# Kernel optimization log

Measured on AMD Instinct MI355X. Metric: run time of the kernel, lower is better.

Reference implementation:

```python
import jax, jax.numpy as jnp
import numpy as np

DIM = 768
NUM_HEADS = 12
MLP_RATIO = 4.0
HIDDEN = int(DIM * MLP_RATIO)
EPS = 1e-6  # flax LayerNorm default


def setup_inputs() -> dict:
    key = jax.random.key(0)
    ks = jax.random.split(key, 8)
    d = DIM
    init = lambda k, shape, fan_in: jax.random.normal(k, shape, jnp.float32) * (fan_in ** -0.5)
    return {
        "x": jax.random.normal(ks[0], (8, 1024, d), jnp.float32),
        "ln1_scale": jnp.ones((d,), jnp.float32),
        "ln1_bias": jnp.zeros((d,), jnp.float32),
        "qkv_w": init(ks[1], (d, 3 * d), d),
        "qkv_b": jnp.zeros((3 * d,), jnp.float32),
        "proj_w": init(ks[2], (d, d), d),
        "proj_b": jnp.zeros((d,), jnp.float32),
        "ln2_scale": jnp.ones((d,), jnp.float32),
        "ln2_bias": jnp.zeros((d,), jnp.float32),
        "fc1_w": init(ks[3], (d, HIDDEN), d),
        "fc1_b": jnp.zeros((HIDDEN,), jnp.float32),
        "fc2_w": init(ks[4], (HIDDEN, d), HIDDEN),
        "fc2_b": jnp.zeros((d,), jnp.float32),
    }


def _layernorm(x, scale, bias):
    mu = jnp.mean(x, axis=-1, keepdims=True)
    var = jnp.mean(jnp.square(x - mu), axis=-1, keepdims=True)
    return (x - mu) * jax.lax.rsqrt(var + EPS) * scale + bias


def reference(x, ln1_scale, ln1_bias, qkv_w, qkv_b, proj_w, proj_b,
              ln2_scale, ln2_bias, fc1_w, fc1_b, fc2_w, fc2_b):
    b, n, d = x.shape
    h = NUM_HEADS
    hd = d // h
    scale = hd ** -0.5

    # --- attention (pre-norm) ---
    y = _layernorm(x, ln1_scale, ln1_bias)
    qkv = y @ qkv_w + qkv_b                      # [b, n, 3d]
    qkv = qkv.reshape(b, n, 3, h, hd).transpose(2, 0, 3, 1, 4)  # [3, b, h, n, hd]
    q, k, v = qkv[0], qkv[1], qkv[2]
    attn = jnp.einsum("bhqd,bhkd->bhqk", q, k) * scale
    attn = jax.nn.softmax(attn, axis=-1)
    o = jnp.einsum("bhqk,bhkd->bhqd", attn, v)   # [b, h, n, hd]
    o = o.transpose(0, 2, 1, 3).reshape(b, n, d)
    x = x + (o @ proj_w + proj_b)

    # --- MLP (pre-norm) ---
    y = _layernorm(x, ln2_scale, ln2_bias)
    y = jax.nn.gelu(y @ fc1_w + fc1_b)
    x = x + (y @ fc2_w + fc2_b)
    return x
```

## Files before the change

### kernel.cpp

```cpp
#include <hip/hip_runtime.h>
#include <hip/hip_bf16.h>
#include <math.h>


#define DIM 768
#define SEQ 1024
#define BATCH 8
#define NHEAD 12
#define HDIM 64
#define HID 3072
#define MTOK (BATCH * SEQ)

typedef __attribute__((ext_vector_type(8))) short short8;
typedef __attribute__((ext_vector_type(4))) short short4v;
typedef __attribute__((ext_vector_type(4))) float floatx4;

__device__ __forceinline__ short f2s(float x) {
  __hip_bfloat16 h = __float2bfloat16(x);
  return __builtin_bit_cast(short, h);
}
__device__ __forceinline__ float s2f(short s) {
  return __bfloat162float(__builtin_bit_cast(__hip_bfloat16, s));
}
__device__ __forceinline__ floatx4 zf4() {
  floatx4 v; v[0] = v[1] = v[2] = v[3] = 0.f; return v;
}
__device__ __forceinline__ float gelu_f(float x) {
  float z = 0.7978845608028654f * (x + 0.044715f * x * x * x);
  float u = __expf(2.f * z);
  return 0.5f * x * (2.f - 2.f / (u + 1.f));
}

__global__ __launch_bounds__(256) void pre_kernel(
    const float* __restrict__ w0, short* __restrict__ o0,
    const float* __restrict__ w1, short* __restrict__ o1,
    const float* __restrict__ w2, short* __restrict__ o2,
    const float* __restrict__ w3, short* __restrict__ o3,
    const float* __restrict__ x, const float* __restrict__ ls,
    const float* __restrict__ lb, short* __restrict__ y) {
  const int id = blockIdx.x;
  const int t = threadIdx.x;
  if (id < 6912) {
    __shared__ float tile[32][33];
    const float* in;
    short* out;
    int K, N, tid;
    if (id < 1728)      { in = w0; out = o0; K = DIM; N = 3 * DIM; tid = id; }
    else if (id < 2304) { in = w1; out = o1; K = DIM; N = DIM;     tid = id - 1728; }
    else if (id < 4608) { in = w2; out = o2; K = DIM; N = HID;     tid = id - 2304; }
    else                { in = w3; out = o3; K = HID; N = DIM;     tid = id - 4608; }
    const int ntx = N >> 5;
    const int n0 = (tid % ntx) * 32, k0 = (tid / ntx) * 32;
    const int tx = t & 31, ty = t >> 5;
#pragma unroll
    for (int i = 0; i < 4; ++i)
      tile[ty + i * 8][tx] = in[(size_t)(k0 + ty + i * 8) * N + n0 + tx];
    __syncthreads();
#pragma unroll
    for (int i = 0; i < 4; ++i)
      out[(size_t)(n0 + ty + i * 8) * K + k0 + tx] = f2s(tile[tx][ty + i * 8]);
  } else {
    const int row = id - 6912;
    const float* xr = x + (size_t)row * DIM;
    float v[3];
    float s1 = 0.f, s2 = 0.f;
#pragma unroll
    for (int j = 0; j < 3; ++j) {
      v[j] = xr[t + j * 256];
      s1 += v[j];
      s2 += v[j] * v[j];
    }
#pragma unroll
    for (int off = 32; off; off >>= 1) {
      s1 += __shfl_down(s1, off, 64);
      s2 += __shfl_down(s2, off, 64);
    }
    __shared__ float r1[4], r2[4], bc[2];
    const int wave = t >> 6, lane = t & 63;
    if (lane == 0) { r1[wave] = s1; r2[wave] = s2; }
    __syncthreads();
    if (t == 0) {
      float S1 = r1[0] + r1[1] + r1[2] + r1[3];
      float S2 = r2[0] + r2[1] + r2[2] + r2[3];
      float mu = S1 * (1.0f / DIM);
      float var = S2 * (1.0f / DIM) - mu * mu;
      bc[0] = mu;
      bc[1] = rsqrtf(fmaxf(var, 0.f) + 1e-6f);
    }
    __syncthreads();
    const float mu = bc[0], rstd = bc[1];
#pragma unroll
    for (int j = 0; j < 3; ++j) {
      const int idx = t + j * 256;
      y[(size_t)row * DIM + idx] = f2s((v[j] - mu) * rstd * ls[idx] + lb[idx]);
    }
  }
}

__global__ __launch_bounds__(256) void ln_kernel(const float* __restrict__ x,
                                                 const float* __restrict__ scale,
                                                 const float* __restrict__ bias,
                                                 short* __restrict__ y) {
  const int row = blockIdx.x;
  const int t = threadIdx.x;
  const float* xr = x + (size_t)row * DIM;
  float v[3];
  float s1 = 0.f, s2 = 0.f;
#pragma unroll
  for (int j = 0; j < 3; ++j) {
    v[j] = xr[t + j * 256];
    s1 += v[j];
    s2 += v[j] * v[j];
  }
#pragma unroll
  for (int off = 32; off; off >>= 1) {
    s1 += __shfl_down(s1, off, 64);
    s2 += __shfl_down(s2, off, 64);
  }
  __shared__ float r1[4], r2[4], bc[2];
  const int wave = t >> 6, lane = t & 63;
  if (lane == 0) { r1[wave] = s1; r2[wave] = s2; }
  __syncthreads();
  if (t == 0) {
    float S1 = r1[0] + r1[1] + r1[2] + r1[3];
    float S2 = r2[0] + r2[1] + r2[2] + r2[3];
    float mu = S1 * (1.0f / DIM);
    float var = S2 * (1.0f / DIM) - mu * mu;
    bc[0] = mu;
    bc[1] = rsqrtf(fmaxf(var, 0.f) + 1e-6f);
  }
  __syncthreads();
  const float mu = bc[0], rstd = bc[1];
#pragma unroll
  for (int j = 0; j < 3; ++j) {
    const int idx = t + j * 256;
    y[(size_t)row * DIM + idx] = f2s((v[j] - mu) * rstd * scale[idx] + bias[idx]);
  }
}

template <int ROWS, int THREADS>
__device__ __forceinline__ void stageT(const short* __restrict__ src, int ld,
                                       short* lds, int t) {
#pragma unroll
  for (int i = 0; i < (ROWS * 4) / THREADS; ++i) {
    const int S = i * THREADS + t;
    const int row = S >> 2;
    const int chunk = (S & 3) ^ ((row >> 1) & 3);
    const short* g = src + (size_t)row * ld + chunk * 8;
    const unsigned off = __builtin_amdgcn_readfirstlane((unsigned)((S & ~63) * 16));
    __builtin_amdgcn_global_load_lds(
        (const __attribute__((address_space(1))) void*)g,
        (__attribute__((address_space(3))) void*)((char*)lds + off), 16, 0, 0);
  }
}

template <int MODE>
__global__ __launch_bounds__(256) void gemm_w192(
    const short* __restrict__ A, const short* __restrict__ Bt,
    const float* __restrict__ bias,
    short* __restrict__ outB,
    short* __restrict__ Qb, short* __restrict__ Kb, short* __restrict__ Vtb,
    int N, int K) {
  __shared__ __align__(16) short Asm[4][4096];
  __shared__ __align__(16) short Bsm[4][6144];
  const int t = threadIdx.x;
  const int lane = t & 63, w = t >> 6, quad = lane >> 4, l15 = lane & 15;

  const int nbx = gridDim.x;
  const int lid = blockIdx.y * nbx + blockIdx.x;
  const int xcd = lid & 7, local = lid >> 3;
  const int m0 = ((local / nbx) * 8 + xcd) * 128;
  const int n0 = (local % nbx) * 192;
  const int mb = (w & 1) * 64, nb = (w >> 1) * 96;

  floatx4 acc[4][6];
#pragma unroll
  for (int mi = 0; mi < 4; ++mi)
#pragma unroll
    for (int ni = 0; ni < 6; ++ni) acc[mi][ni] = zf4();

  const short* Ab = A + (size_t)m0 * K;
  const short* Bb = Bt + (size_t)n0 * K;
  const int nk = K >> 5;

  stageT<128, 256>(Ab, K, Asm[0], t);       stageT<192, 256>(Bb, K, Bsm[0], t);
  stageT<128, 256>(Ab + 32, K, Asm[1], t);  stageT<192, 256>(Bb + 32, K, Bsm[1], t);
  stageT<128, 256>(Ab + 64, K, Asm[2], t);  stageT<192, 256>(Bb + 64, K, Bsm[2], t);

#define W192_STEP(BUF) do { \
  short8 a_[4], b_[6]; \
  _Pragma("unroll") for (int mi = 0; mi < 4; ++mi) { \
    const int r = mb + mi * 16 + l15; \
    a_[mi] = *(const short8*)(Asm[BUF] + r * 32 + ((quad ^ ((r >> 1) & 3)) * 8)); \
  } \
  _Pragma("unroll") for (int ni = 0; ni < 6; ++ni) { \
    const int r = nb + ni * 16 + l15; \
    b_[ni] = *(const short8*)(Bsm[BUF] + r * 32 + ((quad ^ ((r >> 1) & 3)) * 8)); \
  } \
  _Pragma("unroll") for (int mi = 0; mi < 4; ++mi) \
    _Pragma("unroll") for (int ni = 0; ni < 6; ++ni) \
      acc[mi][ni] = __builtin_amdgcn_mfma_f32_16x16x32_bf16(a_[mi], b_[ni], acc[mi][ni], 0, 0, 0); \
} while (0)

#define W192_IT(J, BUF, NXT) do { \
  if ((J) + 2 < nk)      asm volatile("s_waitcnt vmcnt(10)" ::: "memory"); \
  else if ((J) + 1 < nk) asm volatile("s_waitcnt vmcnt(5)" ::: "memory"); \
  else                   asm volatile("s_waitcnt vmcnt(0)" ::: "memory"); \
  __builtin_amdgcn_s_barrier(); \
  if ((J) + 3 < nk) { \
    stageT<128, 256>(Ab + ((J) + 3) * 32, K, Asm[NXT], t); \
    stageT<192, 256>(Bb + ((J) + 3) * 32, K, Bsm[NXT], t); \
  } \
  W192_STEP(BUF); \
} while (0)

  for (int kt = 0; kt < nk; kt += 4) {
    W192_IT(kt + 0, 0, 3);
    W192_IT(kt + 1, 1, 0);
    W192_IT(kt + 2, 2, 1);
    W192_IT(kt + 3, 3, 2);
  }

#pragma unroll
  for (int mi = 0; mi < 4; ++mi) {
    const int row0 = m0 + mb + mi * 16 + quad * 4;
#pragma unroll
    for (int ni = 0; ni < 6; ++ni) {
      const int col = n0 + nb + ni * 16 + l15;
      const float bv = bias[col];
      float v[4];
#pragma unroll
      for (int r = 0; r < 4; ++r) v[r] = acc[mi][ni][r] + bv;
      if (MODE == 0) {
        const int bb = row0 >> 10;
        const int s0 = row0 & 1023;
        if (col < 1536) {
          const int cc = (col < 768) ? col : col - 768;
          const int h = cc >> 6, d = cc & 63;
          short* dst = (col < 768 ? Qb : Kb) + (size_t)(bb * NHEAD + h) * SEQ * HDIM;
#pragma unroll
          for (int r = 0; r < 4; ++r) dst[(size_t)(s0 + r) * HDIM + d] = f2s(v[r]);
        } else {
          const int cc = col - 1536;
          const int h = cc >> 6, d = cc & 63;
          short4v pv;
#pragma unroll
          for (int r = 0; r < 4; ++r) pv[r] = f2s(v[r]);
          *(short4v*)(Vtb + ((size_t)(bb * NHEAD + h) * HDIM + d) * SEQ + s0) = pv;
        }
      } else {
#pragma unroll
        for (int r = 0; r < 4; ++r)
          outB[(size_t)(row0 + r) * N + col] = f2s(gelu_f(v[r]));
      }
    }
  }
}

__global__ __launch_bounds__(128) void gemm_n64(
    const short* __restrict__ A, const short* __restrict__ Bt,
    const float* __restrict__ bias, const float* __restrict__ res,
    float* __restrict__ outF, int N, int K) {
  __shared__ __align__(16) short Asm[4][4096];
  __shared__ __align__(16) short Bsm[4][2048];
  const int t = threadIdx.x;
  const int lane = t & 63, w = t >> 6, quad = lane >> 4, l15 = lane & 15;

  const int nbx = gridDim.x;
  const int lid = blockIdx.y * nbx + blockIdx.x;
  const int xcd = lid & 7, local = lid >> 3;
  const int m0 = ((local / nbx) * 8 + xcd) * 128;
  const int n0 = (local % nbx) * 64;
  const int mb = w * 64;

  floatx4 acc[4][4];
#pragma unroll
  for (int mi = 0; mi < 4; ++mi)
#pragma unroll
    for (int ni = 0; ni < 4; ++ni) acc[mi][ni] = zf4();

  const short* Ab = A + (size_t)m0 * K;
  const short* Bb = Bt + (size_t)n0 * K;
  const int nk = K >> 5;

  stageT<128, 128>(Ab, K, Asm[0], t);       stageT<64, 128>(Bb, K, Bsm[0], t);
  stageT<128, 128>(Ab + 32, K, Asm[1], t);  stageT<64, 128>(Bb + 32, K, Bsm[1], t);
  stageT<128, 128>(Ab + 64, K, Asm[2], t);  stageT<64, 128>(Bb + 64, K, Bsm[2], t);

#define N64_STEP(BUF) do { \
  short8 a_[4], b_[4]; \
  _Pragma("unroll") for (int mi = 0; mi < 4; ++mi) { \
    const int r = mb + mi * 16 + l15; \
    a_[mi] = *(const short8*)(Asm[BUF] + r * 32 + ((quad ^ ((r >> 1) & 3)) * 8)); \
  } \
  _Pragma("unroll") for (int ni = 0; ni < 4; ++ni) { \
    const int r = ni * 16 + l15; \
    b_[ni] = *(const short8*)(Bsm[BUF] + r * 32 + ((quad ^ ((r >> 1) & 3)) * 8)); \
  } \
  _Pragma("unroll") for (int mi = 0; mi < 4; ++mi) \
    _Pragma("unroll") for (int ni = 0; ni < 4; ++ni) \
      acc[mi][ni] = __builtin_amdgcn_mfma_f32_16x16x32_bf16(a_[mi], b_[ni], acc[mi][ni], 0, 0, 0); \
} while (0)

#define N64_IT(J, BUF, NXT) do { \
  if ((J) + 2 < nk)      asm volatile("s_waitcnt vmcnt(12)" ::: "memory"); \
  else if ((J) + 1 < nk) asm volatile("s_waitcnt vmcnt(6)" ::: "memory"); \
  else                   asm volatile("s_waitcnt vmcnt(0)" ::: "memory"); \
  __builtin_amdgcn_s_barrier(); \
  if ((J) + 3 < nk) { \
    stageT<128, 128>(Ab + ((J) + 3) * 32, K, Asm[NXT], t); \
    stageT<64, 128>(Bb + ((J) + 3) * 32, K, Bsm[NXT], t); \
  } \
  N64_STEP(BUF); \
} while (0)

  for (int kt = 0; kt < nk; kt += 4) {
    N64_IT(kt + 0, 0, 3);
    N64_IT(kt + 1, 1, 0);
    N64_IT(kt + 2, 2, 1);
    N64_IT(kt + 3, 3, 2);
  }

#pragma unroll
  for (int mi = 0; mi < 4; ++mi) {
    const int row0 = m0 + mb + mi * 16 + quad * 4;
#pragma unroll
    for (int ni = 0; ni < 4; ++ni) {
      const int col = n0 + ni * 16 + l15;
      const float bv = bias[col];
#pragma unroll
      for (int r = 0; r < 4; ++r) {
        const size_t idx = (size_t)(row0 + r) * N + col;
        outF[idx] = acc[mi][ni][r] + bv + res[idx];
      }
    }
  }
}

__device__ __forceinline__ void stage64(const short* __restrict__ src, int ld,
                                        short* lds, int t) {
  const int lane = t & 63, w = t >> 6;
#pragma unroll
  for (int i = 0; i < 2; ++i) {
    const int S = w * 128 + i * 64 + lane;
    const int r = S >> 3, c0 = S & 7;
    const int c = c0 ^ (r & 7);
    const short* g = src + (size_t)r * ld + c * 8;
    const unsigned off = __builtin_amdgcn_readfirstlane((unsigned)((w * 128 + i * 64) * 16));
    __builtin_amdgcn_global_load_lds(
        (const __attribute__((address_space(1))) void*)g,
        (__attribute__((address_space(3))) void*)((char*)lds + off), 16, 0, 0);
  }
}

__global__ __launch_bounds__(256) void attn_kernel(
    const short* __restrict__ Qb, const short* __restrict__ Kb,
    const short* __restrict__ Vtb, short* __restrict__ o) {
  __shared__ __align__(16) short Ks[2][4096];
  __shared__ __align__(16) short Vts[2][4096];
  __shared__ __align__(16) short Pt[8192];
  const int t = threadIdx.x;
  const int lane = t & 63, w = t >> 6, quad = lane >> 4, l15 = lane & 15;
  const int bh = blockIdx.x;
  const int q0 = blockIdx.y * 128;
  const size_t qkbase = (size_t)bh * SEQ * HDIM;
  const size_t vbase = (size_t)bh * HDIM * SEQ;
  short* ptw = Pt + w * 2048;
  const float cexp = 0.18033688011f;

  short8 bq[2][2];
#pragma unroll
  for (int mi = 0; mi < 2; ++mi)
#pragma unroll
    for (int ks = 0; ks < 2; ++ks)
      bq[mi][ks] = *(const short8*)(Qb + qkbase +
                                    (size_t)(q0 + w * 32 + mi * 16 + l15) * HDIM +
                                    ks * 32 + quad * 8);

  floatx4 oacc[4][2];
  float l_acc[2] = {0.f, 0.f};
#pragma unroll
  for (int di = 0; di < 4; ++di)
#pragma unroll
    for (int mi = 0; mi < 2; ++mi) oacc[di][mi] = zf4();

  stage64(Kb + qkbase, HDIM, Ks[0], t);
  stage64(Vtb + vbase, SEQ, Vts[0], t);

  for (int kt = 0; kt < 16; ++kt) {
    __syncthreads();
    const int cur = kt & 1;
    if (kt < 15) {
      stage64(Kb + qkbase + (size_t)(kt + 1) * 64 * HDIM, HDIM, Ks[cur ^ 1], t);
      stage64(Vtb + vbase + (kt + 1) * 64, SEQ, Vts[cur ^ 1], t);
    }

    floatx4 sacc[4][2];
#pragma unroll
    for (int ni = 0; ni < 4; ++ni)
#pragma unroll
      for (int mi = 0; mi < 2; ++mi) sacc[ni][mi] = zf4();
#pragma unroll
    for (int ks = 0; ks < 2; ++ks) {
      short8 ak[4];
#pragma unroll
      for (int ni = 0; ni < 4; ++ni) {
        const int r = ni * 16 + l15;
        ak[ni] = *(const short8*)(Ks[cur] + r * 64 + (((ks * 4 + quad) ^ (r & 7)) * 8));
      }
#pragma unroll
      for (int ni = 0; ni < 4; ++ni)
#pragma unroll
        for (int mi = 0; mi < 2; ++mi)
          sacc[ni][mi] = __builtin_amdgcn_mfma_f32_16x16x32_bf16(ak[ni], bq[mi][ks], sacc[ni][mi], 0, 0, 0);
    }

#pragma unroll
    for (int mi = 0; mi < 2; ++mi) {
      const int row = mi * 16 + l15;
      const int swz = (row & 7) ^ ((row & 8) >> 1);
#pragma unroll
      for (int ni = 0; ni < 4; ++ni) {
        short4v pk;
#pragma unroll
        for (int r = 0; r < 4; ++r) {
          const float p = exp2f(sacc[ni][mi][r] * cexp);
          l_acc[mi] += p;
          pk[r] = f2s(p);
        }
        const int c = ni * 2 + (quad >> 1);
        *(short4v*)(ptw + row * 64 + ((c ^ swz) * 8 + (quad & 1) * 4)) = pk;
      }
    }

#pragma unroll
    for (int ks = 0; ks < 2; ++ks) {
      short8 bp[2];
#pragma unroll
      for (int mi = 0; mi < 2; ++mi) {
        const int row = mi * 16 + l15;
        const int swz = (row & 7) ^ ((row & 8) >> 1);
        bp[mi] = *(const short8*)(ptw + row * 64 + (((ks * 4 + quad) ^ swz) * 8));
      }
      short8 av[4];
#pragma unroll
      for (int di = 0; di < 4; ++di) {
        const int r = di * 16 + l15;
        av[di] = *(const short8*)(Vts[cur] + r * 64 + (((ks * 4 + quad) ^ (r & 7)) * 8));
      }
#pragma unroll
      for (int di = 0; di < 4; ++di)
#pragma unroll
        for (int mi = 0; mi < 2; ++mi)
          oacc[di][mi] = __builtin_amdgcn_mfma_f32_16x16x32_bf16(av[di], bp[mi], oacc[di][mi], 0, 0, 0);
    }
  }

  const int bb = bh / NHEAD, hh = bh % NHEAD;
  float inv[2];
#pragma unroll
  for (int mi = 0; mi < 2; ++mi) {
    float l = l_acc[mi];
    l += __shfl_xor(l, 16, 64);
    l += __shfl_xor(l, 32, 64);
    inv[mi] = 1.0f / l;
  }
#pragma unroll
  for (int di = 0; di < 4; ++di)
#pragma unroll
    for (int mi = 0; mi < 2; ++mi) {
      const int tok = bb * SEQ + q0 + w * 32 + mi * 16 + l15;
      const int d = hh * HDIM + di * 16 + quad * 4;
      short4v ov;
#pragma unroll
      for (int r = 0; r < 4; ++r) ov[r] = f2s(oacc[di][mi][r] * inv[mi]);
      *(short4v*)(o + (size_t)tok * DIM + d) = ov;
    }
}

extern "C" void kernel_launch(void* const* d_in, const int* in_sizes, int n_in,
                              void* d_out, int out_size, void* d_ws, size_t ws_size,
                              hipStream_t stream) {
  const float* x      = (const float*)d_in[0];
  const float* ln1_s  = (const float*)d_in[1];
  const float* ln1_b  = (const float*)d_in[2];
  const float* qkv_w  = (const float*)d_in[3];
  const float* qkv_b  = (const float*)d_in[4];
  const float* proj_w = (const float*)d_in[5];
  const float* proj_b = (const float*)d_in[6];
  const float* ln2_s  = (const float*)d_in[7];
  const float* ln2_b  = (const float*)d_in[8];
  const float* fc1_w  = (const float*)d_in[9];
  const float* fc1_b  = (const float*)d_in[10];
  const float* fc2_w  = (const float*)d_in[11];
  const float* fc2_b  = (const float*)d_in[12];
  float* out = (float*)d_out;

  char* p = (char*)d_ws;
  short* wqt = (short*)p; p += (size_t)(3 * DIM) * DIM * 2;
  short* wpt = (short*)p; p += (size_t)DIM * DIM * 2;
  short* w1t = (short*)p; p += (size_t)HID * DIM * 2;
  short* w2t = (short*)p; p += (size_t)DIM * HID * 2;
  short* y   = (short*)p; p += (size_t)MTOK * DIM * 2;
  short* Qb  = (short*)p; p += (size_t)MTOK * DIM * 2;
  short* Kb  = (short*)p; p += (size_t)MTOK * DIM * 2;
  short* Vtb = (short*)p; p += (size_t)MTOK * DIM * 2;
  float* x1  = (float*)p; p += (size_t)MTOK * DIM * 4;
  short* h   = (short*)p; p += (size_t)MTOK * HID * 2;
  short* obuf = y;
  short* y2   = Qb;

  pre_kernel<<<6912 + MTOK, 256, 0, stream>>>(qkv_w, wqt, proj_w, wpt, fc1_w, w1t,
                                              fc2_w, w2t, x, ln1_s, ln1_b, y);
  gemm_w192<0><<<dim3(12, 64), 256, 0, stream>>>(
      y, wqt, qkv_b, nullptr, Qb, Kb, Vtb, 3 * DIM, DIM);
  attn_kernel<<<dim3(BATCH * NHEAD, SEQ / 128), 256, 0, stream>>>(Qb, Kb, Vtb, obuf);
  gemm_n64<<<dim3(12, 64), 128, 0, stream>>>(
      obuf, wpt, proj_b, x, x1, DIM, DIM);
  ln_kernel<<<MTOK, 256, 0, stream>>>(x1, ln2_s, ln2_b, y2);
  gemm_w192<2><<<dim3(16, 64), 256, 0, stream>>>(
      y2, w1t, fc1_b, h, nullptr, nullptr, nullptr, HID, DIM);
  gemm_n64<<<dim3(12, 64), 128, 0, stream>>>(
      h, w2t, fc2_b, x1, out, DIM, HID);
}
```

Before: 423.1 us.

## Replace LDS-staged GEMM pipelines with direct global-to-register double buffering

Both GEMM kernels drop the four-stage global_load_lds shared-memory pipeline and barriers. Each wave now loads its MFMA fragments directly from global memory into registers, double-buffered across k-steps. This removes LDS usage and block-level synchronization, which may raise occupancy. In exchange, operand tiles shared between waves are fetched redundantly from global/L2, and memory latency is hidden only by a two-deep register prefetch.

```diff
diff --git a/kernel.cpp b/kernel.cpp
--- a/kernel.cpp
+++ b/kernel.cpp
@@ -138,31 +138,13 @@
   }
 }
 
-template <int ROWS, int THREADS>
-__device__ __forceinline__ void stageT(const short* __restrict__ src, int ld,
-                                       short* lds, int t) {
-#pragma unroll
-  for (int i = 0; i < (ROWS * 4) / THREADS; ++i) {
-    const int S = i * THREADS + t;
-    const int row = S >> 2;
-    const int chunk = (S & 3) ^ ((row >> 1) & 3);
-    const short* g = src + (size_t)row * ld + chunk * 8;
-    const unsigned off = __builtin_amdgcn_readfirstlane((unsigned)((S & ~63) * 16));
-    __builtin_amdgcn_global_load_lds(
-        (const __attribute__((address_space(1))) void*)g,
-        (__attribute__((address_space(3))) void*)((char*)lds + off), 16, 0, 0);
-  }
-}
-
 template <int MODE>
-__global__ __launch_bounds__(256) void gemm_w192(
+__global__ __launch_bounds__(256) void gemm_reg192(
     const short* __restrict__ A, const short* __restrict__ Bt,
     const float* __restrict__ bias,
     short* __restrict__ outB,
     short* __restrict__ Qb, short* __restrict__ Kb, short* __restrict__ Vtb,
     int N, int K) {
-  __shared__ __align__(16) short Asm[4][4096];
-  __shared__ __align__(16) short Bsm[4][6144];
   const int t = threadIdx.x;
   const int lane = t & 63, w = t >> 6, quad = lane >> 4, l15 = lane & 15;
 
@@ -173,52 +155,42 @@
   const int n0 = (local % nbx) * 192;
   const int mb = (w & 1) * 64, nb = (w >> 1) * 96;
 
+  const short* pa[4];
+  const short* pb[6];
+#pragma unroll
+  for (int mi = 0; mi < 4; ++mi)
+    pa[mi] = A + (size_t)(m0 + mb + mi * 16 + l15) * K + quad * 8;
+#pragma unroll
+  for (int ni = 0; ni < 6; ++ni)
+    pb[ni] = Bt + (size_t)(n0 + nb + ni * 16 + l15) * K + quad * 8;
+
   floatx4 acc[4][6];
 #pragma unroll
   for (int mi = 0; mi < 4; ++mi)
 #pragma unroll
     for (int ni = 0; ni < 6; ++ni) acc[mi][ni] = zf4();
 
-  const short* Ab = A + (size_t)m0 * K;
-  const short* Bb = Bt + (size_t)n0 * K;
-  const int nk = K >> 5;
-
-  stageT<128, 256>(Ab, K, Asm[0], t);       stageT<192, 256>(Bb, K, Bsm[0], t);
-  stageT<128, 256>(Ab + 32, K, Asm[1], t);  stageT<192, 256>(Bb + 32, K, Bsm[1], t);
-  stageT<128, 256>(Ab + 64, K, Asm[2], t);  stageT<192, 256>(Bb + 64, K, Bsm[2], t);
-
-#define W192_STEP(BUF) do { \
-  short8 a_[4], b_[6]; \
-  _Pragma("unroll") for (int mi = 0; mi < 4; ++mi) { \
-    const int r = mb + mi * 16 + l15; \
-    a_[mi] = *(const short8*)(Asm[BUF] + r * 32 + ((quad ^ ((r >> 1) & 3)) * 8)); \
-  } \
-  _Pragma("unroll") for (int ni = 0; ni < 6; ++ni) { \
-    const int r = nb + ni * 16 + l15; \
-    b_[ni] = *(const short8*)(Bsm[BUF] + r * 32 + ((quad ^ ((r >> 1) & 3)) * 8)); \
-  } \
+#define R192_LOAD(AD, BD, KOFF) do { \
+  _Pragma("unroll") for (int mi = 0; mi < 4; ++mi) \
+    AD[mi] = *(const short8*)(pa[mi] + (KOFF)); \
+  _Pragma("unroll") for (int ni = 0; ni < 6; ++ni) \
+    BD[ni] = *(const short8*)(pb[ni] + (KOFF)); \
+} while (0)
+
+#define R192_MFMA(AD, BD) do { \
   _Pragma("unroll") for (int mi = 0; mi < 4; ++mi) \
     _Pragma("unroll") for (int ni = 0; ni < 6; ++ni) \
-      acc[mi][ni] = __builtin_amdgcn_mfma_f32_16x16x32_bf16(a_[mi], b_[ni], acc[mi][ni], 0, 0, 0); \
+      acc[mi][ni] = __builtin_amdgcn_mfma_f32_16x16x32_bf16(AD[mi], BD[ni], acc[mi][ni], 0, 0, 0); \
 } while (0)
 
-#define W192_IT(J, BUF, NXT) do { \
-  if ((J) + 2 < nk)      asm volatile("s_waitcnt vmcnt(10)" ::: "memory"); \
-  else if ((J) + 1 < nk) asm volatile("s_waitcnt vmcnt(5)" ::: "memory"); \
-  else                   asm volatile("s_waitcnt vmcnt(0)" ::: "memory"); \
-  __builtin_amdgcn_s_barrier(); \
-  if ((J) + 3 < nk) { \
-    stageT<128, 256>(Ab + ((J) + 3) * 32, K, Asm[NXT], t); \
-    stageT<192, 256>(Bb + ((J) + 3) * 32, K, Bsm[NXT], t); \
-  } \
-  W192_STEP(BUF); \
-} while (0)
-
-  for (int kt = 0; kt < nk; kt += 4) {
-    W192_IT(kt + 0, 0, 3);
-    W192_IT(kt + 1, 1, 0);
-    W192_IT(kt + 2, 2, 1);
-    W192_IT(kt + 3, 3, 2);
+  short8 a0[4], b0[6], a1[4], b1[6];
+  R192_LOAD(a0, b0, 0);
+  const int nk = K >> 5;
+  for (int kt = 0; kt < nk; kt += 2) {
+    R192_LOAD(a1, b1, (kt + 1) * 32);
+    R192_MFMA(a0, b0);
+    if (kt + 2 < nk) R192_LOAD(a0, b0, (kt + 2) * 32);
+    R192_MFMA(a1, b1);
   }
 
 #pragma unroll
@@ -257,12 +229,10 @@
   }
 }
 
-__global__ __launch_bounds__(128) void gemm_n64(
+__global__ __launch_bounds__(128) void gemm_reg64(
     const short* __restrict__ A, const short* __restrict__ Bt,
     const float* __restrict__ bias, const float* __restrict__ res,
     float* __restrict__ outF, int N, int K) {
-  __shared__ __align__(16) short Asm[4][4096];
-  __shared__ __align__(16) short Bsm[4][2048];
   const int t = threadIdx.x;
   const int lane = t & 63, w = t >> 6, quad = lane >> 4, l15 = lane & 15;
 
@@ -273,52 +243,42 @@
   const int n0 = (local % nbx) * 64;
   const int mb = w * 64;
 
+  const short* pa[4];
+  const short* pb[4];
+#pragma unroll
+  for (int mi = 0; mi < 4; ++mi)
+    pa[mi] = A + (size_t)(m0 + mb + mi * 16 + l15) * K + quad * 8;
+#pragma unroll
+  for (int ni = 0; ni < 4; ++ni)
+    pb[ni] = Bt + (size_t)(n0 + ni * 16 + l15) * K + quad * 8;
+
   floatx4 acc[4][4];
 #pragma unroll
   for (int mi = 0; mi < 4; ++mi)
 #pragma unroll
     for (int ni = 0; ni < 4; ++ni) acc[mi][ni] = zf4();
 
-  const short* Ab = A + (size_t)m0 * K;
-  const short* Bb = Bt + (size_t)n0 * K;
-  const int nk = K >> 5;
-
-  stageT<128, 128>(Ab, K, Asm[0], t);       stageT<64, 128>(Bb, K, Bsm[0], t);
-  stageT<128, 128>(Ab + 32, K, Asm[1], t);  stageT<64, 128>(Bb + 32, K, Bsm[1], t);
-  stageT<128, 128>(Ab + 64, K, Asm[2], t);  stageT<64, 128>(Bb + 64, K, Bsm[2], t);
-
-#define N64_STEP(BUF) do { \
-  short8 a_[4], b_[4]; \
-  _Pragma("unroll") for (int mi = 0; mi < 4; ++mi) { \
-    const int r = mb + mi * 16 + l15; \
-    a_[mi] = *(const short8*)(Asm[BUF] + r * 32 + ((quad ^ ((r >> 1) & 3)) * 8)); \
-  } \
-  _Pragma("unroll") for (int ni = 0; ni < 4; ++ni) { \
-    const int r = ni * 16 + l15; \
-    b_[ni] = *(const short8*)(Bsm[BUF] + r * 32 + ((quad ^ ((r >> 1) & 3)) * 8)); \
-  } \
+#define R64_LOAD(AD, BD, KOFF) do { \
+  _Pragma("unroll") for (int mi = 0; mi < 4; ++mi) \
+    AD[mi] = *(const short8*)(pa[mi] + (KOFF)); \
+  _Pragma("unroll") for (int ni = 0; ni < 4; ++ni) \
+    BD[ni] = *(const short8*)(pb[ni] + (KOFF)); \
+} while (0)
+
+#define R64_MFMA(AD, BD) do { \
   _Pragma("unroll") for (int mi = 0; mi < 4; ++mi) \
     _Pragma("unroll") for (int ni = 0; ni < 4; ++ni) \
-      acc[mi][ni] = __builtin_amdgcn_mfma_f32_16x16x32_bf16(a_[mi], b_[ni], acc[mi][ni], 0, 0, 0); \
+      acc[mi][ni] = __builtin_amdgcn_mfma_f32_16x16x32_bf16(AD[mi], BD[ni], acc[mi][ni], 0, 0, 0); \
 } while (0)
 
-#define N64_IT(J, BUF, NXT) do { \
-  if ((J) + 2 < nk)      asm volatile("s_waitcnt vmcnt(12)" ::: "memory"); \
-  else if ((J) + 1 < nk) asm volatile("s_waitcnt vmcnt(6)" ::: "memory"); \
-  else                   asm volatile("s_waitcnt vmcnt(0)" ::: "memory"); \
-  __builtin_amdgcn_s_barrier(); \
-  if ((J) + 3 < nk) { \
-    stageT<128, 128>(Ab + ((J) + 3) * 32, K, Asm[NXT], t); \
-    stageT<64, 128>(Bb + ((J) + 3) * 32, K, Bsm[NXT], t); \
-  } \
-  N64_STEP(BUF); \
-} while (0)
-
-  for (int kt = 0; kt < nk; kt += 4) {
-    N64_IT(kt + 0, 0, 3);
-    N64_IT(kt + 1, 1, 0);
-    N64_IT(kt + 2, 2, 1);
-    N64_IT(kt + 3, 3, 2);
+  short8 a0[4], b0[4], a1[4], b1[4];
+  R64_LOAD(a0, b0, 0);
+  const int nk = K >> 5;
+  for (int kt = 0; kt < nk; kt += 2) {
+    R64_LOAD(a1, b1, (kt + 1) * 32);
+    R64_MFMA(a0, b0);
+    if (kt + 2 < nk) R64_LOAD(a0, b0, (kt + 2) * 32);
+    R64_MFMA(a1, b1);
   }
 
 #pragma unroll
@@ -512,14 +472,14 @@
 
   pre_kernel<<<6912 + MTOK, 256, 0, stream>>>(qkv_w, wqt, proj_w, wpt, fc1_w, w1t,
                                               fc2_w, w2t, x, ln1_s, ln1_b, y);
-  gemm_w192<0><<<dim3(12, 64), 256, 0, stream>>>(
+  gemm_reg192<0><<<dim3(12, 64), 256, 0, stream>>>(
       y, wqt, qkv_b, nullptr, Qb, Kb, Vtb, 3 * DIM, DIM);
   attn_kernel<<<dim3(BATCH * NHEAD, SEQ / 128), 256, 0, stream>>>(Qb, Kb, Vtb, obuf);
-  gemm_n64<<<dim3(12, 64), 128, 0, stream>>>(
+  gemm_reg64<<<dim3(12, 64), 128, 0, stream>>>(
       obuf, wpt, proj_b, x, x1, DIM, DIM);
   ln_kernel<<<MTOK, 256, 0, stream>>>(x1, ln2_s, ln2_b, y2);
-  gemm_w192<2><<<dim3(16, 64), 256, 0, stream>>>(
+  gemm_reg192<2><<<dim3(16, 64), 256, 0, stream>>>(
       y2, w1t, fc1_b, h, nullptr, nullptr, nullptr, HID, DIM);
-  gemm_n64<<<dim3(12, 64), 128, 0, stream>>>(
+  gemm_reg64<<<dim3(12, 64), 128, 0, stream>>>(
       h, w2t, fc2_b, x1, out, DIM, HID);
 }
```

After: 598.1 us. 41.4% more time.
